# Kernel optimization log

Hardware: AMD Instinct MI355X
Metric: run time of the kernel (lower is better)

## Reference

```python
import jax, jax.numpy as jnp
import numpy as np

N_NODES = 50000
N_EDGES = 1500000
MEM_DIM = 128
EFEAT_DIM = 128
TEMP_DIM = 100


def setup_inputs() -> dict:
    key = jax.random.key(0)
    ks = jax.random.split(key, 10)
    src = jax.random.randint(ks[0], (N_EDGES,), 0, N_NODES)
    dst = jax.random.randint(ks[1], (N_EDGES,), 0, N_NODES)
    edge_ts = jax.random.uniform(ks[2], (N_EDGES,), dtype=jnp.float32) * 100.0
    edge_feats = jax.random.normal(ks[3], (N_EDGES, EFEAT_DIM), dtype=jnp.float32)
    mem_s = jax.random.normal(ks[4], (N_NODES, MEM_DIM), dtype=jnp.float32)
    last_update_t = jax.random.uniform(ks[5], (N_NODES,), dtype=jnp.float32) * 50.0
    # TimeEncode: deterministic init, w = 1/10**linspace(0,9,dim), bias zeros
    time_w = jnp.asarray(1.0 / 10 ** np.linspace(0, 9, TEMP_DIM), dtype=jnp.float32)
    time_b = jnp.zeros((TEMP_DIM,), dtype=jnp.float32)
    msg_dim = MEM_DIM + MEM_DIM + EFEAT_DIM + TEMP_DIM  # 484
    W_ih = jax.random.normal(ks[6], (3 * MEM_DIM, msg_dim), dtype=jnp.float32) * 0.05
    W_hh = jax.random.normal(ks[7], (3 * MEM_DIM, MEM_DIM), dtype=jnp.float32) * 0.05
    b_ih = jax.random.normal(ks[8], (3 * MEM_DIM,), dtype=jnp.float32) * 0.05
    b_hh = jax.random.normal(ks[9], (3 * MEM_DIM,), dtype=jnp.float32) * 0.05
    return {"src": src, "dst": dst, "edge_ts": edge_ts, "edge_feats": edge_feats,
            "mem_s": mem_s, "last_update_t": last_update_t,
            "time_w": time_w, "time_b": time_b,
            "W_ih": W_ih, "W_hh": W_hh, "b_ih": b_ih, "b_hh": b_hh}


def reference(src, dst, edge_ts, edge_feats, mem_s, last_update_t,
              time_w, time_b, W_ih, W_hh, b_ih, b_hh):
    N, H = mem_s.shape
    E = src.shape[0]
    # --- agg_last: per-dst node, pick the incoming edge with max timestamp ---
    max_ts = jax.ops.segment_max(edge_ts, dst, num_segments=N)  # -inf if no msgs
    is_max = edge_ts == max_ts[dst]
    eidx = jnp.arange(E)
    win = jax.ops.segment_max(jnp.where(is_max, eidx, -1), dst, num_segments=N)
    has_msg = win >= 0  # [N]
    w = jnp.clip(win, 0)  # safe index for empty nodes (masked later)
    # --- msg_fn_cat, computed only for the winning edge per node ---
    src_w = src[w]  # [N]
    delta = edge_ts[w] - last_update_t[src_w]  # [N]
    tenc = jnp.cos(delta[:, None] * time_w[None, :] + time_b[None, :])  # [N,T]
    # winning edge's dst == node itself, so edges.dst['s'] == mem_s
    m_bar = jnp.concatenate([mem_s[src_w], mem_s, edge_feats[w], tenc], axis=1)  # [N,484]
    # --- GRUCell(m_bar, mem_s) ---
    gi = m_bar @ W_ih.T + b_ih  # [N, 3H]
    gh = mem_s @ W_hh.T + b_hh  # [N, 3H]
    i_r, i_z, i_n = jnp.split(gi, 3, axis=1)
    h_r, h_z, h_n = jnp.split(gh, 3, axis=1)
    r = jax.nn.sigmoid(i_r + h_r)
    z = jax.nn.sigmoid(i_z + h_z)
    n = jnp.tanh(i_n + r * h_n)
    h_new = (1.0 - z) * n + z * mem_s
    # only nodes that received messages are updated by update_all
    s_out = jnp.where(has_msg[:, None], h_new, mem_s)
    ts_out = jnp.where(has_msg, max_ts, last_update_t)
    return s_out, ts_out
```

## Files before the change

kernel.cpp:

```cpp
#include <hip/hip_runtime.h>
#include <stdint.h>
#include <math.h>

#define N_NODES 50000
#define N_EDGES 1500000
#define HDIM 128
#define TDIM 100
#define KPAD 512
#define BM 64
#define NT 512
#define NBLOCKS ((N_NODES + BM - 1) / BM)

typedef __attribute__((ext_vector_type(8))) short short8v;
typedef __attribute__((ext_vector_type(4))) float f32x4;
typedef __attribute__((ext_vector_type(4))) unsigned int u32x4;

__device__ __forceinline__ unsigned short f2bf(float x) {
    unsigned int u = __float_as_uint(x);
    return (unsigned short)((u + 0x7fffu + ((u >> 16) & 1u)) >> 16);
}
__device__ __forceinline__ float bf2f(unsigned short b) {
    return __uint_as_float((unsigned)b << 16);
}
__device__ __forceinline__ float sigmoidf_(float x) { return 1.0f / (1.0f + __expf(-x)); }
__device__ __forceinline__ float tanhf_(float x) { return 2.0f / (1.0f + __expf(-2.0f * x)) - 1.0f; }

__global__ void scan_edges_kernel(const int* __restrict__ dst,
                                  const float* __restrict__ edge_ts,
                                  unsigned long long* __restrict__ keys) {
    int e = blockIdx.x * 256 + threadIdx.x;
    if (e < N_EDGES) {
        unsigned tsb = __float_as_uint(__builtin_nontemporal_load(&edge_ts[e]));
        int d = __builtin_nontemporal_load(&dst[e]);
        unsigned cur_hi = ((const unsigned*)keys)[2 * d + 1];
        if (tsb >= cur_hi) {
            unsigned long long key =
                ((unsigned long long)tsb << 32) | (unsigned int)(e + 1);
            atomicMax(&keys[d], key);
        }
    }
}

__global__ void convert_w_kernel(const float* __restrict__ Wih, const float* __restrict__ Whh,
                                 unsigned short* __restrict__ wbF1, unsigned short* __restrict__ wbF2) {
    int t = blockIdx.x * 256 + threadIdx.x;
    if (t < 24576) {
        int b = t >> 10, kt = (t >> 6) & 15, l = t & 63;
        int g3 = b >> 3, n8 = b & 7;
        int srow = g3 * 128 + n8 * 16 + (l & 15);
        int scol = kt * 32 + (l >> 4) * 8;
        unsigned short v[8];
        #pragma unroll
        for (int j = 0; j < 8; ++j)
            v[j] = (scol + j < 484) ? f2bf(Wih[srow * 484 + scol + j]) : (unsigned short)0;
        uint4 pk;
        pk.x = (unsigned)v[0] | ((unsigned)v[1] << 16);
        pk.y = (unsigned)v[2] | ((unsigned)v[3] << 16);
        pk.z = (unsigned)v[4] | ((unsigned)v[5] << 16);
        pk.w = (unsigned)v[6] | ((unsigned)v[7] << 16);
        *(uint4*)&wbF1[(size_t)t * 8] = pk;
    } else if (t < 24576 + 6144) {
        int t2 = t - 24576;
        int b = t2 >> 8, kt = (t2 >> 6) & 3, l = t2 & 63;
        int g3 = b >> 3, n8 = b & 7;
        int srow = g3 * 128 + n8 * 16 + (l & 15);
        int scol = kt * 32 + (l >> 4) * 8;
        unsigned short v[8];
        #pragma unroll
        for (int j = 0; j < 8; ++j) v[j] = f2bf(Whh[srow * 128 + scol + j]);
        uint4 pk;
        pk.x = (unsigned)v[0] | ((unsigned)v[1] << 16);
        pk.y = (unsigned)v[2] | ((unsigned)v[3] << 16);
        pk.z = (unsigned)v[4] | ((unsigned)v[5] << 16);
        pk.w = (unsigned)v[6] | ((unsigned)v[7] << 16);
        *(uint4*)&wbF2[(size_t)t2 * 8] = pk;
    }
}

__global__ __launch_bounds__(NT, 4)
void gru_mfma_kernel(const int* __restrict__ src,
                     const float* __restrict__ edge_ts,
                     const float* __restrict__ ef,
                     const float* __restrict__ mem,
                     const float* __restrict__ lut,
                     const float* __restrict__ tw,
                     const float* __restrict__ tb,
                     const float* __restrict__ bih,
                     const float* __restrict__ bhh,
                     const unsigned short* __restrict__ wbF1,
                     const unsigned short* __restrict__ wbF2,
                     const unsigned long long* __restrict__ keys,
                     float* __restrict__ out) {
    __shared__ unsigned short Alds[BM * KPAD];
    __shared__ unsigned char sh_has[BM];
    const int tid = threadIdx.x;
    const int base = blockIdx.x * BM;

    {
        const int i = tid >> 3, l8 = tid & 7;
        const int n = base + i;
        if (n < N_NODES) {
            unsigned long long key = keys[n];
            const int has = (key != 0ULL);
            const int e = has ? (int)((unsigned)key - 1u) : 0;
            const int s = src[e];
            const float tv = edge_ts[e];
            const float d = tv - lut[s];
            if (l8 == 0) {
                sh_has[i] = (unsigned char)has;
                __builtin_nontemporal_store(has ? tv : lut[n],
                                            &out[(size_t)N_NODES * HDIM + n]);
            }
            const int swg = i & 7;
            unsigned short* Arow = &Alds[i * KPAD];
            #pragma unroll
            for (int p = 0; p < 8; ++p) {
                const int gk = p * 8 + l8, k0 = gk * 8;
                float f[8];
                if (k0 < 384) {
                    const float* sp = (k0 < 128) ? mem + (size_t)s * HDIM + k0
                                    : (k0 < 256) ? mem + (size_t)n * HDIM + (k0 - 128)
                                                 : ef + (size_t)e * HDIM + (k0 - 256);
                    u32x4 w0 = __builtin_nontemporal_load((const u32x4*)sp);
                    u32x4 w1 = __builtin_nontemporal_load((const u32x4*)sp + 1);
                    f[0]=__uint_as_float(w0.x); f[1]=__uint_as_float(w0.y);
                    f[2]=__uint_as_float(w0.z); f[3]=__uint_as_float(w0.w);
                    f[4]=__uint_as_float(w1.x); f[5]=__uint_as_float(w1.y);
                    f[6]=__uint_as_float(w1.z); f[7]=__uint_as_float(w1.w);
                } else {
                    #pragma unroll
                    for (int j2 = 0; j2 < 8; ++j2) {
                        int q = k0 - 384 + j2;
                        f[j2] = (q < TDIM) ? cosf(fmaf(d, tw[q], tb[q])) : 0.f;
                    }
                }
                uint4 pk;
                pk.x = (unsigned)f2bf(f[0]) | ((unsigned)f2bf(f[1]) << 16);
                pk.y = (unsigned)f2bf(f[2]) | ((unsigned)f2bf(f[3]) << 16);
                pk.z = (unsigned)f2bf(f[4]) | ((unsigned)f2bf(f[5]) << 16);
                pk.w = (unsigned)f2bf(f[6]) | ((unsigned)f2bf(f[7]) << 16);
                *(uint4*)&Arow[(size_t)(gk ^ swg) * 8] = pk;
            }
        }
    }
    __syncthreads();

    const int n8 = tid >> 6, l = tid & 63;
    const int lr = l & 15, lh = l >> 4;

    const short8v* Bv1 = (const short8v*)wbF1 + l;
    const short8v* Bv2 = (const short8v*)wbF2 + l;

    const f32x4 fzero = {0.f, 0.f, 0.f, 0.f};
    f32x4 acc[4][4];
    #pragma unroll
    for (int q = 0; q < 4; ++q)
        #pragma unroll
        for (int mf = 0; mf < 4; ++mf) acc[q][mf] = fzero;

    #pragma unroll 2
    for (int kt = 0; kt < 16; ++kt) {
        short8v b[3];
        #pragma unroll
        for (int g3 = 0; g3 < 3; ++g3)
            b[g3] = Bv1[((g3 * 8 + n8) * 16 + kt) * 64];
        short8v a[4];
        #pragma unroll
        for (int mf = 0; mf < 4; ++mf) {
            const int row = mf * 16 + lr;
            a[mf] = *(const short8v*)&Alds[row * KPAD + ((kt * 32 + lh * 8) ^ ((row & 7) << 3))];
        }
        #pragma unroll
        for (int g3 = 0; g3 < 3; ++g3)
            #pragma unroll
            for (int mf = 0; mf < 4; ++mf)
                acc[g3][mf] = __builtin_amdgcn_mfma_f32_16x16x32_bf16(
                    a[mf], b[g3], acc[g3][mf], 0, 0, 0);
    }
    #pragma unroll 2
    for (int kt = 0; kt < 4; ++kt) {
        short8v b[3];
        #pragma unroll
        for (int g3 = 0; g3 < 3; ++g3)
            b[g3] = Bv2[((g3 * 8 + n8) * 4 + kt) * 64];
        short8v a[4];
        #pragma unroll
        for (int mf = 0; mf < 4; ++mf) {
            const int row = mf * 16 + lr;
            a[mf] = *(const short8v*)&Alds[row * KPAD + (((128 + kt * 32) + lh * 8) ^ ((row & 7) << 3))];
        }
        #pragma unroll
        for (int g3 = 0; g3 < 3; ++g3) {
            const int q = (g3 < 2) ? g3 : 3;
            #pragma unroll
            for (int mf = 0; mf < 4; ++mf)
                acc[q][mf] = __builtin_amdgcn_mfma_f32_16x16x32_bf16(
                    a[mf], b[g3], acc[q][mf], 0, 0, 0);
        }
    }

    const int c = n8 * 16 + lr;
    const float br = bih[c] + bhh[c];
    const float bz = bih[HDIM + c] + bhh[HDIM + c];
    const float bin = bih[2 * HDIM + c];
    const float bhn = bhh[2 * HDIM + c];
    const int hg = 16 + (c >> 3);
    const int ho = c & 7;
    #pragma unroll
    for (int mf = 0; mf < 4; ++mf)
        #pragma unroll
        for (int ii = 0; ii < 4; ++ii) {
            const int row = mf * 16 + lh * 4 + ii;
            const int node = base + row;
            if (node >= N_NODES) continue;
            if (!sh_has[row]) continue;
            const float r = sigmoidf_(acc[0][mf][ii] + br);
            const float z = sigmoidf_(acc[1][mf][ii] + bz);
            const float ng = tanhf_(acc[2][mf][ii] + bin + r * (acc[3][mf][ii] + bhn));
            const float h = bf2f(Alds[row * KPAD + (hg ^ (row & 7)) * 8 + ho]);
            __builtin_nontemporal_store((1.f - z) * ng + z * h,
                                        &out[(size_t)node * HDIM + c]);
        }
}

extern "C" void kernel_launch(void* const* d_in, const int* in_sizes, int n_in,
                              void* d_out, int out_size, void* d_ws, size_t ws_size,
                              hipStream_t stream) {
    const int* src       = (const int*)d_in[0];
    const int* dst       = (const int*)d_in[1];
    const float* edge_ts = (const float*)d_in[2];
    const float* ef      = (const float*)d_in[3];
    const float* mem     = (const float*)d_in[4];
    const float* lut     = (const float*)d_in[5];
    const float* tw      = (const float*)d_in[6];
    const float* tb      = (const float*)d_in[7];
    const float* Wih     = (const float*)d_in[8];
    const float* Whh     = (const float*)d_in[9];
    const float* bih     = (const float*)d_in[10];
    const float* bhh     = (const float*)d_in[11];
    float* out = (float*)d_out;

    char* ws = (char*)d_ws;
    unsigned long long* keys = (unsigned long long*)ws;
    unsigned short* wbF1 = (unsigned short*)(ws + 524288);
    unsigned short* wbF2 = (unsigned short*)(ws + 917504);

    hipMemsetAsync(keys, 0, (size_t)N_NODES * 8, stream);
    scan_edges_kernel<<<(N_EDGES + 255) / 256, 256, 0, stream>>>(dst, edge_ts, keys);
    convert_w_kernel<<<(24576 + 6144 + 255) / 256, 256, 0, stream>>>(Wih, Whh, wbF1, wbF2);
    hipMemcpyAsync(out, mem, (size_t)N_NODES * HDIM * sizeof(float),
                   hipMemcpyDeviceToDevice, stream);
    gru_mfma_kernel<<<NBLOCKS, NT, 0, stream>>>(
        src, edge_ts, ef, mem, lut, tw, tb, bih, bhh, wbF1, wbF2, keys, out);
}
```

Measured before the change: 139.9 us.

## Switch GRU GEMM to FP8 MFMA with folded W_hh r/z weights

```diff
diff --git a/kernel.cpp b/kernel.cpp
--- a/kernel.cpp
+++ b/kernel.cpp
@@ -11,19 +11,19 @@
 #define NT 512
 #define NBLOCKS ((N_NODES + BM - 1) / BM)
 
-typedef __attribute__((ext_vector_type(8))) short short8v;
+typedef long long ll_t;
+typedef __attribute__((ext_vector_type(2))) ll_t ll2v;
 typedef __attribute__((ext_vector_type(4))) float f32x4;
 typedef __attribute__((ext_vector_type(4))) unsigned int u32x4;
 
-__device__ __forceinline__ unsigned short f2bf(float x) {
-    unsigned int u = __float_as_uint(x);
-    return (unsigned short)((u + 0x7fffu + ((u >> 16) & 1u)) >> 16);
-}
-__device__ __forceinline__ float bf2f(unsigned short b) {
-    return __uint_as_float((unsigned)b << 16);
-}
 __device__ __forceinline__ float sigmoidf_(float x) { return 1.0f / (1.0f + __expf(-x)); }
 __device__ __forceinline__ float tanhf_(float x) { return 2.0f / (1.0f + __expf(-2.0f * x)) - 1.0f; }
+
+__device__ __forceinline__ unsigned pk8(float a, float b, float c, float d) {
+    unsigned v = __builtin_amdgcn_cvt_pk_fp8_f32(a, b, 0, false);
+    v = __builtin_amdgcn_cvt_pk_fp8_f32(c, d, (int)v, true);
+    return v;
+}
 
 __global__ void scan_edges_kernel(const int* __restrict__ dst,
                                   const float* __restrict__ edge_ts,
@@ -42,38 +42,44 @@
 }
 
 __global__ void convert_w_kernel(const float* __restrict__ Wih, const float* __restrict__ Whh,
-                                 unsigned short* __restrict__ wbF1, unsigned short* __restrict__ wbF2) {
+                                 unsigned char* __restrict__ wbF1p,
+                                 unsigned char* __restrict__ wbF2p) {
     int t = blockIdx.x * 256 + threadIdx.x;
-    if (t < 24576) {
-        int b = t >> 10, kt = (t >> 6) & 15, l = t & 63;
-        int g3 = b >> 3, n8 = b & 7;
-        int srow = g3 * 128 + n8 * 16 + (l & 15);
-        int scol = kt * 32 + (l >> 4) * 8;
-        unsigned short v[8];
-        #pragma unroll
-        for (int j = 0; j < 8; ++j)
-            v[j] = (scol + j < 484) ? f2bf(Wih[srow * 484 + scol + j]) : (unsigned short)0;
-        uint4 pk;
-        pk.x = (unsigned)v[0] | ((unsigned)v[1] << 16);
-        pk.y = (unsigned)v[2] | ((unsigned)v[3] << 16);
-        pk.z = (unsigned)v[4] | ((unsigned)v[5] << 16);
-        pk.w = (unsigned)v[6] | ((unsigned)v[7] << 16);
-        *(uint4*)&wbF1[(size_t)t * 8] = pk;
-    } else if (t < 24576 + 6144) {
-        int t2 = t - 24576;
-        int b = t2 >> 8, kt = (t2 >> 6) & 3, l = t2 & 63;
-        int g3 = b >> 3, n8 = b & 7;
-        int srow = g3 * 128 + n8 * 16 + (l & 15);
-        int scol = kt * 32 + (l >> 4) * 8;
-        unsigned short v[8];
-        #pragma unroll
-        for (int j = 0; j < 8; ++j) v[j] = f2bf(Whh[srow * 128 + scol + j]);
-        uint4 pk;
-        pk.x = (unsigned)v[0] | ((unsigned)v[1] << 16);
-        pk.y = (unsigned)v[2] | ((unsigned)v[3] << 16);
-        pk.z = (unsigned)v[4] | ((unsigned)v[5] << 16);
-        pk.w = (unsigned)v[6] | ((unsigned)v[7] << 16);
-        *(uint4*)&wbF2[(size_t)t2 * 8] = pk;
+    if (t < 12288) {
+        const int bidx = t >> 9, ktp = (t >> 6) & 7, l = t & 63;
+        const int g3 = bidx >> 3, n8 = bidx & 7;
+        const int row = g3 * 128 + n8 * 16 + (l & 15);
+        unsigned q[4];
+        #pragma unroll
+        for (int h2 = 0; h2 < 2; ++h2) {
+            const int kbase = (2 * ktp + h2) * 32 + (l >> 4) * 8;
+            float f[8];
+            #pragma unroll
+            for (int j = 0; j < 8; ++j) {
+                const int k = kbase + j;
+                float w = (k < 484) ? Wih[row * 484 + k] : 0.f;
+                if (g3 < 2 && k >= 128 && k < 256) w += Whh[row * 128 + (k - 128)];
+                f[j] = w;
+            }
+            q[2 * h2]     = pk8(f[0], f[1], f[2], f[3]);
+            q[2 * h2 + 1] = pk8(f[4], f[5], f[6], f[7]);
+        }
+        *(u32x4*)&wbF1p[(size_t)t * 16] = (u32x4){q[0], q[1], q[2], q[3]};
+    } else if (t < 12288 + 1024) {
+        const int t2 = t - 12288;
+        const int n8 = t2 >> 7, ktp2 = (t2 >> 6) & 1, l = t2 & 63;
+        const int row = 256 + n8 * 16 + (l & 15);
+        unsigned q[4];
+        #pragma unroll
+        for (int h2 = 0; h2 < 2; ++h2) {
+            const int kbase = (2 * ktp2 + h2) * 32 + (l >> 4) * 8;
+            float f[8];
+            #pragma unroll
+            for (int j = 0; j < 8; ++j) f[j] = Whh[row * 128 + kbase + j];
+            q[2 * h2]     = pk8(f[0], f[1], f[2], f[3]);
+            q[2 * h2 + 1] = pk8(f[4], f[5], f[6], f[7]);
+        }
+        *(u32x4*)&wbF2p[(size_t)t2 * 16] = (u32x4){q[0], q[1], q[2], q[3]};
     }
 }
 
@@ -87,11 +93,11 @@
                      const float* __restrict__ tb,
                      const float* __restrict__ bih,
                      const float* __restrict__ bhh,
-                     const unsigned short* __restrict__ wbF1,
-                     const unsigned short* __restrict__ wbF2,
+                     const unsigned char* __restrict__ wbF1p,
+                     const unsigned char* __restrict__ wbF2p,
                      const unsigned long long* __restrict__ keys,
                      float* __restrict__ out) {
-    __shared__ unsigned short Alds[BM * KPAD];
+    __shared__ unsigned char Alds8[BM * KPAD];
     __shared__ unsigned char sh_has[BM];
     const int tid = threadIdx.x;
     const int base = blockIdx.x * BM;
@@ -111,35 +117,37 @@
                 __builtin_nontemporal_store(has ? tv : lut[n],
                                             &out[(size_t)N_NODES * HDIM + n]);
             }
-            const int swg = i & 7;
-            unsigned short* Arow = &Alds[i * KPAD];
-            #pragma unroll
-            for (int p = 0; p < 8; ++p) {
-                const int gk = p * 8 + l8, k0 = gk * 8;
-                float f[8];
+            const int mf = i >> 4, lrr = i & 15;
+            #pragma unroll
+            for (int p = 0; p < 4; ++p) {
+                const int gk = p * 8 + l8, k0 = gk * 16;
+                float f[16];
                 if (k0 < 384) {
                     const float* sp = (k0 < 128) ? mem + (size_t)s * HDIM + k0
                                     : (k0 < 256) ? mem + (size_t)n * HDIM + (k0 - 128)
                                                  : ef + (size_t)e * HDIM + (k0 - 256);
-                    u32x4 w0 = __builtin_nontemporal_load((const u32x4*)sp);
-                    u32x4 w1 = __builtin_nontemporal_load((const u32x4*)sp + 1);
-                    f[0]=__uint_as_float(w0.x); f[1]=__uint_as_float(w0.y);
-                    f[2]=__uint_as_float(w0.z); f[3]=__uint_as_float(w0.w);
-                    f[4]=__uint_as_float(w1.x); f[5]=__uint_as_float(w1.y);
-                    f[6]=__uint_as_float(w1.z); f[7]=__uint_as_float(w1.w);
+                    #pragma unroll
+                    for (int v = 0; v < 4; ++v) {
+                        u32x4 w = __builtin_nontemporal_load((const u32x4*)sp + v);
+                        f[4*v+0] = __uint_as_float(w.x); f[4*v+1] = __uint_as_float(w.y);
+                        f[4*v+2] = __uint_as_float(w.z); f[4*v+3] = __uint_as_float(w.w);
+                    }
                 } else {
                     #pragma unroll
-                    for (int j2 = 0; j2 < 8; ++j2) {
+                    for (int j2 = 0; j2 < 16; ++j2) {
                         int q = k0 - 384 + j2;
                         f[j2] = (q < TDIM) ? cosf(fmaf(d, tw[q], tb[q])) : 0.f;
                     }
                 }
-                uint4 pk;
-                pk.x = (unsigned)f2bf(f[0]) | ((unsigned)f2bf(f[1]) << 16);
-                pk.y = (unsigned)f2bf(f[2]) | ((unsigned)f2bf(f[3]) << 16);
-                pk.z = (unsigned)f2bf(f[4]) | ((unsigned)f2bf(f[5]) << 16);
-                pk.w = (unsigned)f2bf(f[6]) | ((unsigned)f2bf(f[7]) << 16);
-                *(uint4*)&Arow[(size_t)(gk ^ swg) * 8] = pk;
+                unsigned q0 = pk8(f[0], f[1], f[2], f[3]);
+                unsigned q1 = pk8(f[4], f[5], f[6], f[7]);
+                unsigned q2 = pk8(f[8], f[9], f[10], f[11]);
+                unsigned q3 = pk8(f[12], f[13], f[14], f[15]);
+                const int kt = k0 >> 5, ktp = kt >> 1, half = kt & 1;
+                const int lh0 = (k0 & 31) >> 3;
+                const int a1 = (mf * 8 + ktp) * 1024 + (lh0 * 16 + lrr) * 16 + half * 8;
+                *(uint2*)&Alds8[a1]       = (uint2){q0, q1};
+                *(uint2*)&Alds8[a1 + 256] = (uint2){q2, q3};
             }
         }
     }
@@ -148,8 +156,9 @@
     const int n8 = tid >> 6, l = tid & 63;
     const int lr = l & 15, lh = l >> 4;
 
-    const short8v* Bv1 = (const short8v*)wbF1 + l;
-    const short8v* Bv2 = (const short8v*)wbF2 + l;
+    const ll2v* Alv = (const ll2v*)Alds8;
+    const ll2v* Bv1 = (const ll2v*)wbF1p;
+    const ll2v* Bv2 = (const ll2v*)wbF2p;
 
     const f32x4 fzero = {0.f, 0.f, 0.f, 0.f};
     f32x4 acc[4][4];
@@ -159,43 +168,38 @@
         for (int mf = 0; mf < 4; ++mf) acc[q][mf] = fzero;
 
     #pragma unroll 2
-    for (int kt = 0; kt < 16; ++kt) {
-        short8v b[3];
+    for (int ktp = 0; ktp < 8; ++ktp) {
+        ll2v b[3];
         #pragma unroll
         for (int g3 = 0; g3 < 3; ++g3)
-            b[g3] = Bv1[((g3 * 8 + n8) * 16 + kt) * 64];
-        short8v a[4];
+            b[g3] = Bv1[((g3 * 8 + n8) * 8 + ktp) * 64 + l];
+        ll2v a[4];
+        #pragma unroll
+        for (int mf = 0; mf < 4; ++mf)
+            a[mf] = Alv[(mf * 8 + ktp) * 64 + l];
+        #pragma unroll
+        for (int g3 = 0; g3 < 3; ++g3)
+            #pragma unroll
+            for (int mf = 0; mf < 4; ++mf) {
+                acc[g3][mf] = __builtin_amdgcn_mfma_f32_16x16x32_fp8_fp8(
+                    a[mf].x, b[g3].x, acc[g3][mf], 0, 0, 0);
+                acc[g3][mf] = __builtin_amdgcn_mfma_f32_16x16x32_fp8_fp8(
+                    a[mf].y, b[g3].y, acc[g3][mf], 0, 0, 0);
+            }
+    }
+    #pragma unroll
+    for (int ktp2 = 0; ktp2 < 2; ++ktp2) {
+        ll2v b2 = Bv2[(n8 * 2 + ktp2) * 64 + l];
+        ll2v a[4];
+        #pragma unroll
+        for (int mf = 0; mf < 4; ++mf)
+            a[mf] = Alv[(mf * 8 + 2 + ktp2) * 64 + l];
         #pragma unroll
         for (int mf = 0; mf < 4; ++mf) {
-            const int row = mf * 16 + lr;
-            a[mf] = *(const short8v*)&Alds[row * KPAD + ((kt * 32 + lh * 8) ^ ((row & 7) << 3))];
-        }
-        #pragma unroll
-        for (int g3 = 0; g3 < 3; ++g3)
-            #pragma unroll
-            for (int mf = 0; mf < 4; ++mf)
-                acc[g3][mf] = __builtin_amdgcn_mfma_f32_16x16x32_bf16(
-                    a[mf], b[g3], acc[g3][mf], 0, 0, 0);
-    }
-    #pragma unroll 2
-    for (int kt = 0; kt < 4; ++kt) {
-        short8v b[3];
-        #pragma unroll
-        for (int g3 = 0; g3 < 3; ++g3)
-            b[g3] = Bv2[((g3 * 8 + n8) * 4 + kt) * 64];
-        short8v a[4];
-        #pragma unroll
-        for (int mf = 0; mf < 4; ++mf) {
-            const int row = mf * 16 + lr;
-            a[mf] = *(const short8v*)&Alds[row * KPAD + (((128 + kt * 32) + lh * 8) ^ ((row & 7) << 3))];
-        }
-        #pragma unroll
-        for (int g3 = 0; g3 < 3; ++g3) {
-            const int q = (g3 < 2) ? g3 : 3;
-            #pragma unroll
-            for (int mf = 0; mf < 4; ++mf)
-                acc[q][mf] = __builtin_amdgcn_mfma_f32_16x16x32_bf16(
-                    a[mf], b[g3], acc[q][mf], 0, 0, 0);
+            acc[3][mf] = __builtin_amdgcn_mfma_f32_16x16x32_fp8_fp8(
+                a[mf].x, b2.x, acc[3][mf], 0, 0, 0);
+            acc[3][mf] = __builtin_amdgcn_mfma_f32_16x16x32_fp8_fp8(
+                a[mf].y, b2.y, acc[3][mf], 0, 0, 0);
         }
     }
 
@@ -204,8 +208,8 @@
     const float bz = bih[HDIM + c] + bhh[HDIM + c];
     const float bin = bih[2 * HDIM + c];
     const float bhn = bhh[2 * HDIM + c];
-    const int hg = 16 + (c >> 3);
-    const int ho = c & 7;
+    const int kh = 128 + c;
+    const int kth = kh >> 5, ktph = kth >> 1, halfh = kth & 1, lhk = (kh & 31) >> 3;
     #pragma unroll
     for (int mf = 0; mf < 4; ++mf)
         #pragma unroll
@@ -217,7 +221,9 @@
             const float r = sigmoidf_(acc[0][mf][ii] + br);
             const float z = sigmoidf_(acc[1][mf][ii] + bz);
             const float ng = tanhf_(acc[2][mf][ii] + bin + r * (acc[3][mf][ii] + bhn));
-            const float h = bf2f(Alds[row * KPAD + (hg ^ (row & 7)) * 8 + ho]);
+            const int hoff = (mf * 8 + ktph) * 1024 + (lhk * 16 + (row & 15)) * 16
+                             + halfh * 8 + (kh & 7);
+            const float h = __builtin_amdgcn_cvt_f32_fp8((int)Alds8[hoff], 0);
             __builtin_nontemporal_store((1.f - z) * ng + z * h,
                                         &out[(size_t)node * HDIM + c]);
         }
@@ -242,14 +248,14 @@
 
     char* ws = (char*)d_ws;
     unsigned long long* keys = (unsigned long long*)ws;
-    unsigned short* wbF1 = (unsigned short*)(ws + 524288);
-    unsigned short* wbF2 = (unsigned short*)(ws + 917504);
+    unsigned char* wbF1p = (unsigned char*)(ws + 524288);
+    unsigned char* wbF2p = (unsigned char*)(ws + 524288 + 196608);
 
     hipMemsetAsync(keys, 0, (size_t)N_NODES * 8, stream);
     scan_edges_kernel<<<(N_EDGES + 255) / 256, 256, 0, stream>>>(dst, edge_ts, keys);
-    convert_w_kernel<<<(24576 + 6144 + 255) / 256, 256, 0, stream>>>(Wih, Whh, wbF1, wbF2);
+    convert_w_kernel<<<(12288 + 1024 + 255) / 256, 256, 0, stream>>>(Wih, Whh, wbF1p, wbF2p);
     hipMemcpyAsync(out, mem, (size_t)N_NODES * HDIM * sizeof(float),
                    hipMemcpyDeviceToDevice, stream);
     gru_mfma_kernel<<<NBLOCKS, NT, 0, stream>>>(
-        src, edge_ts, ef, mem, lut, tw, tb, bih, bhh, wbF1, wbF2, keys, out);
-}
+        src, edge_ts, ef, mem, lut, tw, tb, bih, bhh, wbF1p, wbF2p, keys, out);
+}
```

New measurement: 145.2 us. 1.04x slower.

## Fold W_hh r/z into W_ih, drop output memcpy, stage stores via LDS

Applied to the files above, without the earlier changes.

```diff
diff --git a/kernel.cpp b/kernel.cpp
--- a/kernel.cpp
+++ b/kernel.cpp
@@ -10,6 +10,7 @@
 #define BM 64
 #define NT 512
 #define NBLOCKS ((N_NODES + BM - 1) / BM)
+#define OPITCH 130
 
 typedef __attribute__((ext_vector_type(8))) short short8v;
 typedef __attribute__((ext_vector_type(4))) float f32x4;
@@ -42,32 +43,36 @@
 }
 
 __global__ void convert_w_kernel(const float* __restrict__ Wih, const float* __restrict__ Whh,
-                                 unsigned short* __restrict__ wbF1, unsigned short* __restrict__ wbF2) {
+                                 unsigned short* __restrict__ wbF1,
+                                 unsigned short* __restrict__ wbF2) {
     int t = blockIdx.x * 256 + threadIdx.x;
     if (t < 24576) {
-        int b = t >> 10, kt = (t >> 6) & 15, l = t & 63;
-        int g3 = b >> 3, n8 = b & 7;
-        int srow = g3 * 128 + n8 * 16 + (l & 15);
-        int scol = kt * 32 + (l >> 4) * 8;
+        const int b = t >> 10, kt = (t >> 6) & 15, l = t & 63;
+        const int g3 = b >> 3, n8 = b & 7;
+        const int row = g3 * 128 + n8 * 16 + (l & 15);
+        const int scol = kt * 32 + (l >> 4) * 8;
         unsigned short v[8];
         #pragma unroll
-        for (int j = 0; j < 8; ++j)
-            v[j] = (scol + j < 484) ? f2bf(Wih[srow * 484 + scol + j]) : (unsigned short)0;
+        for (int j = 0; j < 8; ++j) {
+            const int k = scol + j;
+            float w = (k < 484) ? Wih[row * 484 + k] : 0.f;
+            if (g3 < 2 && k >= 128 && k < 256) w += Whh[row * 128 + (k - 128)];
+            v[j] = f2bf(w);
+        }
         uint4 pk;
         pk.x = (unsigned)v[0] | ((unsigned)v[1] << 16);
         pk.y = (unsigned)v[2] | ((unsigned)v[3] << 16);
         pk.z = (unsigned)v[4] | ((unsigned)v[5] << 16);
         pk.w = (unsigned)v[6] | ((unsigned)v[7] << 16);
         *(uint4*)&wbF1[(size_t)t * 8] = pk;
-    } else if (t < 24576 + 6144) {
-        int t2 = t - 24576;
-        int b = t2 >> 8, kt = (t2 >> 6) & 3, l = t2 & 63;
-        int g3 = b >> 3, n8 = b & 7;
-        int srow = g3 * 128 + n8 * 16 + (l & 15);
-        int scol = kt * 32 + (l >> 4) * 8;
+    } else if (t < 24576 + 2048) {
+        const int t2 = t - 24576;
+        const int n8 = t2 >> 8, kt = (t2 >> 6) & 3, l = t2 & 63;
+        const int row = 256 + n8 * 16 + (l & 15);
+        const int scol = kt * 32 + (l >> 4) * 8;
         unsigned short v[8];
         #pragma unroll
-        for (int j = 0; j < 8; ++j) v[j] = f2bf(Whh[srow * 128 + scol + j]);
+        for (int j = 0; j < 8; ++j) v[j] = f2bf(Whh[row * 128 + scol + j]);
         uint4 pk;
         pk.x = (unsigned)v[0] | ((unsigned)v[1] << 16);
         pk.y = (unsigned)v[2] | ((unsigned)v[3] << 16);
@@ -108,8 +113,7 @@
             const float d = tv - lut[s];
             if (l8 == 0) {
                 sh_has[i] = (unsigned char)has;
-                __builtin_nontemporal_store(has ? tv : lut[n],
-                                            &out[(size_t)N_NODES * HDIM + n]);
+                out[(size_t)N_NODES * HDIM + n] = has ? tv : lut[n];
             }
             const int swg = i & 7;
             unsigned short* Arow = &Alds[i * KPAD];
@@ -177,12 +181,9 @@
                 acc[g3][mf] = __builtin_amdgcn_mfma_f32_16x16x32_bf16(
                     a[mf], b[g3], acc[g3][mf], 0, 0, 0);
     }
-    #pragma unroll 2
+    #pragma unroll
     for (int kt = 0; kt < 4; ++kt) {
-        short8v b[3];
-        #pragma unroll
-        for (int g3 = 0; g3 < 3; ++g3)
-            b[g3] = Bv2[((g3 * 8 + n8) * 4 + kt) * 64];
+        short8v b2 = Bv2[(n8 * 4 + kt) * 64];
         short8v a[4];
         #pragma unroll
         for (int mf = 0; mf < 4; ++mf) {
@@ -190,13 +191,9 @@
             a[mf] = *(const short8v*)&Alds[row * KPAD + (((128 + kt * 32) + lh * 8) ^ ((row & 7) << 3))];
         }
         #pragma unroll
-        for (int g3 = 0; g3 < 3; ++g3) {
-            const int q = (g3 < 2) ? g3 : 3;
-            #pragma unroll
-            for (int mf = 0; mf < 4; ++mf)
-                acc[q][mf] = __builtin_amdgcn_mfma_f32_16x16x32_bf16(
-                    a[mf], b[g3], acc[q][mf], 0, 0, 0);
-        }
+        for (int mf = 0; mf < 4; ++mf)
+            acc[3][mf] = __builtin_amdgcn_mfma_f32_16x16x32_bf16(
+                a[mf], b2, acc[3][mf], 0, 0, 0);
     }
 
     const int c = n8 * 16 + lr;
@@ -206,21 +203,38 @@
     const float bhn = bhh[2 * HDIM + c];
     const int hg = 16 + (c >> 3);
     const int ho = c & 7;
+    float o[4][4];
     #pragma unroll
     for (int mf = 0; mf < 4; ++mf)
         #pragma unroll
         for (int ii = 0; ii < 4; ++ii) {
             const int row = mf * 16 + lh * 4 + ii;
-            const int node = base + row;
-            if (node >= N_NODES) continue;
-            if (!sh_has[row]) continue;
+            const float h = bf2f(Alds[row * KPAD + (hg ^ (row & 7)) * 8 + ho]);
             const float r = sigmoidf_(acc[0][mf][ii] + br);
             const float z = sigmoidf_(acc[1][mf][ii] + bz);
             const float ng = tanhf_(acc[2][mf][ii] + bin + r * (acc[3][mf][ii] + bhn));
-            const float h = bf2f(Alds[row * KPAD + (hg ^ (row & 7)) * 8 + ho]);
-            __builtin_nontemporal_store((1.f - z) * ng + z * h,
-                                        &out[(size_t)node * HDIM + c]);
-        }
+            o[mf][ii] = sh_has[row] ? (1.f - z) * ng + z * h : h;
+        }
+    __syncthreads();
+    float* o_lds = (float*)Alds;
+    #pragma unroll
+    for (int mf = 0; mf < 4; ++mf)
+        #pragma unroll
+        for (int ii = 0; ii < 4; ++ii) {
+            const int row = mf * 16 + lh * 4 + ii;
+            o_lds[row * OPITCH + c] = o[mf][ii];
+        }
+    __syncthreads();
+    const int nvalid = (N_NODES - base < BM) ? (N_NODES - base) : BM;
+    #pragma unroll
+    for (int sw = 0; sw < 4; ++sw) {
+        const int idx = sw * 2048 + tid * 4;
+        const int row = idx >> 7, col = idx & 127;
+        if (row < nvalid) {
+            const float4 v = *(const float4*)&o_lds[row * OPITCH + col];
+            *(float4*)&out[(size_t)(base + row) * HDIM + col] = v;
+        }
+    }
 }
 
 extern "C" void kernel_launch(void* const* d_in, const int* in_sizes, int n_in,
@@ -247,9 +261,7 @@
 
     hipMemsetAsync(keys, 0, (size_t)N_NODES * 8, stream);
     scan_edges_kernel<<<(N_EDGES + 255) / 256, 256, 0, stream>>>(dst, edge_ts, keys);
-    convert_w_kernel<<<(24576 + 6144 + 255) / 256, 256, 0, stream>>>(Wih, Whh, wbF1, wbF2);
-    hipMemcpyAsync(out, mem, (size_t)N_NODES * HDIM * sizeof(float),
-                   hipMemcpyDeviceToDevice, stream);
+    convert_w_kernel<<<(24576 + 2048 + 255) / 256, 256, 0, stream>>>(Wih, Whh, wbF1, wbF2);
     gru_mfma_kernel<<<NBLOCKS, NT, 0, stream>>>(
         src, edge_ts, ef, mem, lut, tw, tb, bih, bhh, wbF1, wbF2, keys, out);
 }
```

Result: faster. 129.0 us (-7.8%).
